# Kernel optimization log

Measured on AMD Instinct MI355X. Metric: run time of the kernel, lower is better.

The kernel has to match this reference:

```python
import jax, jax.numpy as jnp
import numpy as np
from jax import lax

NEG = -1000.0  # torch.full((N,S), -1000.0) init in dp_align


def setup_inputs() -> dict:
    key = jax.random.key(0)
    ks = jax.random.split(key, 4)
    N, S, h = 128, 2048, 256          # nodes, segments, hsize
    d = 2 * h                         # bi-LSTM output dim = 2*hsize
    seg_text_feats = jax.random.normal(ks[0], (N, d), jnp.float32)
    vid_feature = jax.random.normal(ks[1], (S, d), jnp.float32)
    # relation_query: Linear(4h, h) -> ReLU -> (Dropout, eval=identity) -> Linear(h, 1)
    W1 = jax.random.normal(ks[2], (h, 2 * d), jnp.float32) / np.sqrt(2.0 * d)
    b1 = jnp.zeros((h,), jnp.float32)
    W2 = jax.random.normal(ks[3], (1, h), jnp.float32) / np.sqrt(float(h))
    b2 = jnp.zeros((1,), jnp.float32)
    return {"seg_text_feats": seg_text_feats, "vid_feature": vid_feature,
            "W1": W1, "b1": b1, "W2": W2, "b2": b2}


def reference(seg_text_feats, vid_feature, W1, b1, W2, b2):
    N, d = seg_text_feats.shape
    S = vid_feature.shape[0]
    # Pairwise MLP logits for every (node, segment) cell, vectorized:
    # concat(text, vid) @ W1^T == text @ W1[:, :d]^T + vid @ W1[:, d:]^T
    A = seg_text_feats @ W1[:, :d].T           # [N, h]
    B = vid_feature @ W1[:, d:].T              # [S, h]
    H = jax.nn.relu(A[:, None, :] + B[None, :, :] + b1)   # [N, S, h]
    logits = jnp.einsum('nsh,h->ns', H, W2[0]) + b2[0]     # [N, S]
    logsig = jax.nn.log_sigmoid(logits)

    n_idx = jnp.arange(N)
    # DP over columns, right to left. prev_col is arr[:, s+1] (virtual col S = NEG).
    def step(prev_col, s):
        ls = logsig[:, s]
        nxt = jnp.concatenate([prev_col[1:], jnp.full((1,), NEG, prev_col.dtype)])  # arr[n+1, s+1]
        curr = ls + jnp.where(n_idx == N - 1, 0.0, nxt)   # last node: no chain term
        take = curr >= prev_col                            # tie -> take current (matches >=)
        val = jnp.where(take, curr, prev_col)
        in_range = (s >= n_idx) & (s <= S - N + n_idx)     # start_ind/end_ind bands
        col = jnp.where(in_range, val, NEG)
        return col, take

    _, takes = lax.scan(step, jnp.full((N,), NEG), jnp.arange(S - 1, -1, -1))
    take_curr = takes[::-1].T                              # [N, S]

    # Backtrack parent pointers from (node 0, segment 0).
    def walk(carry, s):
        n, align = carry
        nc = jnp.minimum(n, N - 1)
        tc = take_curr[nc, s] & (n < N)
        align = align.at[nc].set(jnp.where(tc, s, align[nc]))
        return (n + tc.astype(jnp.int32), align), None

    (_, align), _ = lax.scan(walk, (jnp.int32(0), jnp.zeros((N,), jnp.int32)), jnp.arange(S))

    aggregated_logits = jnp.mean(logits[n_idx, align])     # sum(logit)/num_nodes
    adj_matrix = jnp.zeros((N + S, N + S), jnp.float32).at[S + n_idx, align].set(1.0)
    return adj_matrix, aggregated_logits
```

## Files before the change

kernel.cpp:

```cpp
#include <hip/hip_runtime.h>
#include <math.h>

#define NEGC (-1000.0f)

__global__ __launch_bounds__(256) void k1z_gemm(
    const float* __restrict__ seg, const float* __restrict__ vid,
    const float* __restrict__ W1, const float* __restrict__ b1,
    float* __restrict__ A2, float* __restrict__ B2, float4* __restrict__ out4)
{
    if (blockIdx.x >= 136) {
        const int i = (blockIdx.x - 136) * 256 + threadIdx.x;
        if (i < 1183744) out4[i] = make_float4(0.f, 0.f, 0.f, 0.f);
        return;
    }
    __shared__ float Xs[32][64];
    __shared__ float Ws[32][64];
    const int tid = threadIdx.x;
    const int tx = tid & 15, ty = tid >> 4;
    const int lr = tid >> 2;
    const int lk = (tid & 3) * 8;
    const int colBase = (blockIdx.x & 3) * 64;
    const int rowBase = (blockIdx.x >> 2) * 64;
    const bool isSeg = (rowBase < 128);
    const float* __restrict__ X = isSeg ? seg : vid;
    const int xRow = isSeg ? rowBase : (rowBase - 128);
    const int wOff = isSeg ? 0 : 512;

    float acc[4][4] = {};

    for (int k0 = 0; k0 < 512; k0 += 32) {
        const float* xp = X + (size_t)(xRow + lr) * 512 + (k0 + lk);
        const float4 xa = *(const float4*)xp;
        const float4 xb = *(const float4*)(xp + 4);
        const float* wp = W1 + (size_t)(colBase + lr) * 1024 + (wOff + k0 + lk);
        const float4 wa = *(const float4*)wp;
        const float4 wb = *(const float4*)(wp + 4);
        __syncthreads();
        Xs[lk + 0][lr] = xa.x; Xs[lk + 1][lr] = xa.y;
        Xs[lk + 2][lr] = xa.z; Xs[lk + 3][lr] = xa.w;
        Xs[lk + 4][lr] = xb.x; Xs[lk + 5][lr] = xb.y;
        Xs[lk + 6][lr] = xb.z; Xs[lk + 7][lr] = xb.w;
        Ws[lk + 0][lr] = wa.x; Ws[lk + 1][lr] = wa.y;
        Ws[lk + 2][lr] = wa.z; Ws[lk + 3][lr] = wa.w;
        Ws[lk + 4][lr] = wb.x; Ws[lk + 5][lr] = wb.y;
        Ws[lk + 6][lr] = wb.z; Ws[lk + 7][lr] = wb.w;
        __syncthreads();
        #pragma unroll
        for (int kk = 0; kk < 32; ++kk) {
            const float4 a4 = *(const float4*)&Xs[kk][4 * ty];
            const float4 b4 = *(const float4*)&Ws[kk][4 * tx];
            const float* a = (const float*)&a4;
            const float* b = (const float*)&b4;
            #pragma unroll
            for (int i = 0; i < 4; ++i)
                #pragma unroll
                for (int j = 0; j < 4; ++j)
                    acc[i][j] = fmaf(a[i], b[j], acc[i][j]);
        }
    }

    float* __restrict__ outp = (isSeg ? A2 : B2) + (size_t)xRow * 256;
    const int c = colBase + 4 * tx;
    #pragma unroll
    for (int i = 0; i < 4; ++i) {
        float4 v = make_float4(acc[i][0], acc[i][1], acc[i][2], acc[i][3]);
        if (isSeg) {
            v.x += b1[c + 0]; v.y += b1[c + 1]; v.z += b1[c + 2]; v.w += b1[c + 3];
        }
        *(float4*)(outp + (size_t)(4 * ty + i) * 256 + c) = v;
    }
}

__global__ __launch_bounds__(256) void k2_logits(
    const float* __restrict__ A2, const float* __restrict__ B2,
    const float* __restrict__ W2, const float* __restrict__ b2p,
    float* __restrict__ logitsT, float* __restrict__ lsT)
{
    __shared__ float As[32][64];
    __shared__ float Bs[32][64];
    __shared__ float w2s[256];
    const int tid = threadIdx.x;
    const int tx = tid & 15, ty = tid >> 4;
    const int lr = tid >> 2;
    const int lk = (tid & 3) * 8;
    const int nBase = blockIdx.x * 64;
    const int sBase = blockIdx.y * 64;
    w2s[tid] = W2[tid];
    const float b2v = b2p[0];

    float acc[4][4] = {};

    for (int k0 = 0; k0 < 256; k0 += 32) {
        const float* ap = A2 + (size_t)(nBase + lr) * 256 + (k0 + lk);
        const float4 aa = *(const float4*)ap;
        const float4 ab = *(const float4*)(ap + 4);
        const float* bp = B2 + (size_t)(sBase + lr) * 256 + (k0 + lk);
        const float4 ba = *(const float4*)bp;
        const float4 bb = *(const float4*)(bp + 4);
        __syncthreads();
        As[lk + 0][lr] = aa.x; As[lk + 1][lr] = aa.y;
        As[lk + 2][lr] = aa.z; As[lk + 3][lr] = aa.w;
        As[lk + 4][lr] = ab.x; As[lk + 5][lr] = ab.y;
        As[lk + 6][lr] = ab.z; As[lk + 7][lr] = ab.w;
        Bs[lk + 0][lr] = ba.x; Bs[lk + 1][lr] = ba.y;
        Bs[lk + 2][lr] = ba.z; Bs[lk + 3][lr] = ba.w;
        Bs[lk + 4][lr] = bb.x; Bs[lk + 5][lr] = bb.y;
        Bs[lk + 6][lr] = bb.z; Bs[lk + 7][lr] = bb.w;
        __syncthreads();
        #pragma unroll
        for (int kk = 0; kk < 32; ++kk) {
            const float w = w2s[k0 + kk];
            const float4 a4 = *(const float4*)&As[kk][4 * ty];
            const float4 b4 = *(const float4*)&Bs[kk][4 * tx];
            const float* a = (const float*)&a4;
            const float* b = (const float*)&b4;
            #pragma unroll
            for (int i = 0; i < 4; ++i)
                #pragma unroll
                for (int j = 0; j < 4; ++j)
                    acc[i][j] = fmaf(fmaxf(a[i] + b[j], 0.0f), w, acc[i][j]);
        }
    }

    const int nb = nBase + 4 * ty;
    #pragma unroll
    for (int j = 0; j < 4; ++j) {
        const int s = sBase + 4 * tx + j;
        float4 lg, ls;
        float* lgp = (float*)&lg;
        float* lsp = (float*)&ls;
        #pragma unroll
        for (int i = 0; i < 4; ++i) {
            const float x = acc[i][j] + b2v;
            lgp[i] = x;
            lsp[i] = fminf(x, 0.0f) - log1pf(expf(-fabsf(x)));
        }
        *(float4*)&logitsT[(size_t)s * 128 + nb] = lg;
        *(float4*)&lsT[(size_t)s * 128 + nb] = ls;
    }
}

__global__ __launch_bounds__(64) void k3_dp(
    const float* __restrict__ lsT, const float* __restrict__ logitsT,
    float* __restrict__ out)
{
    __shared__ unsigned takeW[128 * 65];
    __shared__ int alignSh[128];
    const int lane = threadIdx.x;
    const int n0 = 2 * lane, n1 = n0 + 1;
    const float2* __restrict__ ls2 = (const float2*)lsT;

    float p0 = NEGC, p1 = NEGC;
    unsigned u0 = 2047u - (unsigned)n0;
    unsigned u1 = u0 - 1u;
    unsigned w0 = 0u, w1 = 0u;

    auto core = [&](float lx, float ly, float nx) {
        float c0, c1;
        unsigned long long cc;
        asm volatile(
            "v_add_f32 %[c0], %[lx], %[p1]\n\t"
            "v_add_f32 %[c1], %[ly], %[nx]\n\t"
            "v_cmp_ge_f32 vcc, %[c0], %[p0]\n\t"
            "v_cmp_ge_f32 %[cc], %[c1], %[p1]\n\t"
            "v_addc_co_u32 %[w0], vcc, %[w0], %[w0], vcc\n\t"
            "v_addc_co_u32 %[w1], %[cc], %[w1], %[w1], %[cc]\n\t"
            "v_max_f32 %[p0], %[c0], %[p0]\n\t"
            "v_max_f32 %[p1], %[c1], %[p1]\n\t"
            : [p0]"+v"(p0), [p1]"+v"(p1), [w0]"+v"(w0), [w1]"+v"(w1),
              [c0]"=&v"(c0), [c1]"=&v"(c1), [cc]"=&s"(cc)
            : [lx]"v"(lx), [ly]"v"(ly), [nx]"v"(nx)
            : "vcc");
    };

    auto stepF = [&](float2 lsv) {
        float nxt1 = __int_as_float(__builtin_amdgcn_update_dpp(
            0, __float_as_int(p0), 0x130 , 0xf, 0xf, true));
        core(lsv.x, lsv.y, nxt1);
    };
    auto stepM = [&](float2 lsv) {
        float nxt1 = __int_as_float(__builtin_amdgcn_update_dpp(
            0, __float_as_int(p0), 0x130, 0xf, 0xf, true));
        core(lsv.x, lsv.y, nxt1);
        p0 = (u0 <= 1920u) ? p0 : NEGC;
        p1 = (u1 <= 1920u) ? p1 : NEGC;
        --u0; --u1;
    };

    float2 b0[16], b1[16], b2[16], b3[16];
#define LOADG(B, H) { _Pragma("unroll") \
    for (int j = 0; j < 16; ++j) B[j] = ls2[(size_t)((2047 - 16 * (H) - j) * 64 + lane)]; }
#define STEPS_F(B) { _Pragma("unroll") for (int j = 0; j < 16; ++j) stepF(B[j]); }
#define STEPS_M(B) { _Pragma("unroll") for (int j = 0; j < 16; ++j) stepM(B[j]); }
#define FLUSH { takeW[n0 * 65 + wIdx] = w0; takeW[n1 * 65 + wIdx] = w1; \
                w0 = 0u; w1 = 0u; --wIdx; }
#define BODY(SM) \
    LOADG(b3, h + 3); \
    SM(b0); \
    if (h + 4 < 128) LOADG(b0, h + 4); \
    SM(b1); FLUSH; \
    if (h + 5 < 128) LOADG(b1, h + 5); \
    SM(b2); \
    if (h + 6 < 128) LOADG(b2, h + 6); \
    SM(b3); FLUSH;

    LOADG(b0, 0) LOADG(b1, 1) LOADG(b2, 2)
    int wIdx = 63;
    for (int h = 0; h < 8; h += 4) { BODY(STEPS_M) }
    for (int h = 8; h < 120; h += 4) { BODY(STEPS_F) }
    u0 = (unsigned)(127 - n0);
    u1 = u0 - 1u;
    for (int h = 120; h < 128; h += 4) { BODY(STEPS_M) }
#undef BODY
#undef FLUSH
#undef STEPS_M
#undef STEPS_F
#undef LOADG

    alignSh[n0] = 0;
    alignSh[n1] = 0;
    __syncthreads();

    int pos = 0;
    for (int n = 0; n < 128; ++n) {
        unsigned w = takeW[n * 65 + lane];
        const int wi0 = pos >> 5;
        if (lane < wi0) w = 0u;
        else if (lane == wi0) w &= (0xFFFFFFFFu << (pos & 31));
        const unsigned long long m = __ballot(w != 0u);
        if (m == 0ull) break;
        const int fl = __builtin_ctzll(m);
        const unsigned fw = (unsigned)__builtin_amdgcn_readlane((int)w, fl);
        const int s = fl * 32 + __builtin_ctz(fw);
        if (lane == 0) alignSh[n] = s;
        pos = s + 1;
    }
    __syncthreads();

    const int a0 = alignSh[n0];
    const int a1 = alignSh[n1];
    out[(size_t)(2048 + n0) * 2176 + a0] = 1.0f;
    out[(size_t)(2048 + n1) * 2176 + a1] = 1.0f;
    float sum = logitsT[(size_t)a0 * 128 + n0] + logitsT[(size_t)a1 * 128 + n1];
    #pragma unroll
    for (int off = 32; off >= 1; off >>= 1) sum += __shfl_down(sum, off);
    if (lane == 0) out[(size_t)2176 * 2176] = sum * (1.0f / 128.0f);
}

extern "C" void kernel_launch(void* const* d_in, const int* in_sizes, int n_in,
                              void* d_out, int out_size, void* d_ws, size_t ws_size,
                              hipStream_t stream)
{
    const float* seg = (const float*)d_in[0];
    const float* vid = (const float*)d_in[1];
    const float* W1  = (const float*)d_in[2];
    const float* b1  = (const float*)d_in[3];
    const float* W2  = (const float*)d_in[4];
    const float* b2  = (const float*)d_in[5];
    float* out = (float*)d_out;
    float* ws  = (float*)d_ws;

    float* A2      = ws;
    float* B2      = ws + 32768;
    float* logitsT = ws + 557056;
    float* lsT     = ws + 819200;

    k1z_gemm<<<dim3(4760), dim3(256), 0, stream>>>(seg, vid, W1, b1, A2, B2, (float4*)out);
    k2_logits<<<dim3(2, 32), dim3(256), 0, stream>>>(A2, B2, W2, b2, logitsT, lsT);
    k3_dp<<<dim3(1), dim3(64), 0, stream>>>(lsT, logitsT, out);
}
```

Baseline: 197.1 us.

## Pack log-sigmoid values column-pair-wise so the DP loads float4 per lane

```diff
diff --git a/kernel.cpp b/kernel.cpp
--- a/kernel.cpp
+++ b/kernel.cpp
@@ -74,7 +74,7 @@
 __global__ __launch_bounds__(256) void k2_logits(
     const float* __restrict__ A2, const float* __restrict__ B2,
     const float* __restrict__ W2, const float* __restrict__ b2p,
-    float* __restrict__ logitsT, float* __restrict__ lsT)
+    float* __restrict__ logitsT, float* __restrict__ lsPK)
 {
     __shared__ float As[32][64];
     __shared__ float Bs[32][64];
@@ -123,32 +123,42 @@
     }
 
     const int nb = nBase + 4 * ty;
+    const int s0 = sBase + 4 * tx;
+    float lsv[4][4];
     #pragma unroll
     for (int j = 0; j < 4; ++j) {
-        const int s = sBase + 4 * tx + j;
-        float4 lg, ls;
+        const int s = s0 + j;
+        float4 lg;
         float* lgp = (float*)&lg;
-        float* lsp = (float*)&ls;
         #pragma unroll
         for (int i = 0; i < 4; ++i) {
             const float x = acc[i][j] + b2v;
             lgp[i] = x;
-            lsp[i] = fminf(x, 0.0f) - log1pf(expf(-fabsf(x)));
+            lsv[j][i] = fminf(x, 0.0f) - log1pf(expf(-fabsf(x)));
         }
         *(float4*)&logitsT[(size_t)s * 128 + nb] = lg;
-        *(float4*)&lsT[(size_t)s * 128 + nb] = ls;
-    }
-}
-
-__global__ __launch_bounds__(64) void k3_dp(
-    const float* __restrict__ lsT, const float* __restrict__ logitsT,
+    }
+    #pragma unroll
+    for (int m = 0; m < 2; ++m) {
+        const size_t base = (size_t)(s0 / 2 + m) * 256 + 2 * nb;
+        #pragma unroll
+        for (int q = 0; q < 2; ++q) {
+            float4 v = make_float4(lsv[2 * m][2 * q],     lsv[2 * m + 1][2 * q],
+                                   lsv[2 * m][2 * q + 1], lsv[2 * m + 1][2 * q + 1]);
+            *(float4*)&lsPK[base + 4 * q] = v;
+        }
+    }
+}
+
+__global__ __launch_bounds__(64, 1) void k3_dp(
+    const float* __restrict__ lsPK, const float* __restrict__ logitsT,
     float* __restrict__ out)
 {
     __shared__ unsigned takeW[128 * 65];
     __shared__ int alignSh[128];
     const int lane = threadIdx.x;
     const int n0 = 2 * lane, n1 = n0 + 1;
-    const float2* __restrict__ ls2 = (const float2*)lsT;
+    const float4* __restrict__ ls4 = (const float4*)lsPK;
 
     float p0 = NEGC, p1 = NEGC;
     unsigned u0 = 2047u - (unsigned)n0;
@@ -173,44 +183,47 @@
             : "vcc");
     };
 
-    auto stepF = [&](float2 lsv) {
+    auto stepF = [&](float lx, float ly) {
         float nxt1 = __int_as_float(__builtin_amdgcn_update_dpp(
             0, __float_as_int(p0), 0x130 , 0xf, 0xf, true));
-        core(lsv.x, lsv.y, nxt1);
+        core(lx, ly, nxt1);
     };
-    auto stepM = [&](float2 lsv) {
+    auto stepM = [&](float lx, float ly) {
         float nxt1 = __int_as_float(__builtin_amdgcn_update_dpp(
             0, __float_as_int(p0), 0x130, 0xf, 0xf, true));
-        core(lsv.x, lsv.y, nxt1);
+        core(lx, ly, nxt1);
         p0 = (u0 <= 1920u) ? p0 : NEGC;
         p1 = (u1 <= 1920u) ? p1 : NEGC;
         --u0; --u1;
     };
 
-    float2 b0[16], b1[16], b2[16], b3[16];
+    float4 B0[4], B1[4], B2[4], B3[4], B4[4], B5[4], B6[4], B7[4];
 #define LOADG(B, H) { _Pragma("unroll") \
-    for (int j = 0; j < 16; ++j) B[j] = ls2[(size_t)((2047 - 16 * (H) - j) * 64 + lane)]; }
-#define STEPS_F(B) { _Pragma("unroll") for (int j = 0; j < 16; ++j) stepF(B[j]); }
-#define STEPS_M(B) { _Pragma("unroll") for (int j = 0; j < 16; ++j) stepM(B[j]); }
+    for (int j = 0; j < 4; ++j) B[j] = ls4[(size_t)((1023 - 4 * (H) - j) * 64 + lane)]; }
+#define STEPS_F(B) { _Pragma("unroll") \
+    for (int j = 0; j < 4; ++j) { stepF(B[j].y, B[j].w); stepF(B[j].x, B[j].z); } }
+#define STEPS_M(B) { _Pragma("unroll") \
+    for (int j = 0; j < 4; ++j) { stepM(B[j].y, B[j].w); stepM(B[j].x, B[j].z); } }
 #define FLUSH { takeW[n0 * 65 + wIdx] = w0; takeW[n1 * 65 + wIdx] = w1; \
                 w0 = 0u; w1 = 0u; --wIdx; }
 #define BODY(SM) \
-    LOADG(b3, h + 3); \
-    SM(b0); \
-    if (h + 4 < 128) LOADG(b0, h + 4); \
-    SM(b1); FLUSH; \
-    if (h + 5 < 128) LOADG(b1, h + 5); \
-    SM(b2); \
-    if (h + 6 < 128) LOADG(b2, h + 6); \
-    SM(b3); FLUSH;
-
-    LOADG(b0, 0) LOADG(b1, 1) LOADG(b2, 2)
+    SM(B0); if (h +  8 < 256) LOADG(B0, h +  8); \
+    SM(B1); if (h +  9 < 256) LOADG(B1, h +  9); \
+    SM(B2); if (h + 10 < 256) LOADG(B2, h + 10); \
+    SM(B3); FLUSH; if (h + 11 < 256) LOADG(B3, h + 11); \
+    SM(B4); if (h + 12 < 256) LOADG(B4, h + 12); \
+    SM(B5); if (h + 13 < 256) LOADG(B5, h + 13); \
+    SM(B6); if (h + 14 < 256) LOADG(B6, h + 14); \
+    SM(B7); FLUSH; if (h + 15 < 256) LOADG(B7, h + 15);
+
+    LOADG(B0, 0) LOADG(B1, 1) LOADG(B2, 2) LOADG(B3, 3)
+    LOADG(B4, 4) LOADG(B5, 5) LOADG(B6, 6) LOADG(B7, 7)
     int wIdx = 63;
-    for (int h = 0; h < 8; h += 4) { BODY(STEPS_M) }
-    for (int h = 8; h < 120; h += 4) { BODY(STEPS_F) }
+    for (int h = 0; h < 16; h += 8) { BODY(STEPS_M) }
+    for (int h = 16; h < 240; h += 8) { BODY(STEPS_F) }
     u0 = (unsigned)(127 - n0);
     u1 = u0 - 1u;
-    for (int h = 120; h < 128; h += 4) { BODY(STEPS_M) }
+    for (int h = 240; h < 256; h += 8) { BODY(STEPS_M) }
 #undef BODY
 #undef FLUSH
 #undef STEPS_M
@@ -263,9 +276,9 @@
     float* A2      = ws;
     float* B2      = ws + 32768;
     float* logitsT = ws + 557056;
-    float* lsT     = ws + 819200;
+    float* lsPK    = ws + 819200;
 
     k1z_gemm<<<dim3(4760), dim3(256), 0, stream>>>(seg, vid, W1, b1, A2, B2, (float4*)out);
-    k2_logits<<<dim3(2, 32), dim3(256), 0, stream>>>(A2, B2, W2, b2, logitsT, lsT);
-    k3_dp<<<dim3(1), dim3(64), 0, stream>>>(lsT, logitsT, out);
-}
+    k2_logits<<<dim3(2, 32), dim3(256), 0, stream>>>(A2, B2, W2, b2, logitsT, lsPK);
+    k3_dp<<<dim3(1), dim3(64), 0, stream>>>(lsPK, logitsT, out);
+}
```

Result: no change. 193.7 us (-1.7%).
